# Optimization experiments

Hardware: AMD Instinct MI355X
Metric: run time of the kernel (lower is better)

Reference implementation:

```python
import jax, jax.numpy as jnp
import numpy as np

# Config
SEQ_LEN = 512
PRED_LEN = 96
C = 64
TOPM = 4
N_WIRES = 6
PERIODS = [2, 3, 4]          # periods dividing pred_len (model.period_num)
N_SAMPLES = 5000             # size of retrieval table along sample axis
B = 128

# ---- tiny quantum circuit simulation helpers ----
# State vector over n_wires qubits: shape [bsz, 2**n_wires].

def apply_single_qubit_gate(state, gate, wire, n_wires):
    # state: [bsz, 2**n]; gate: [2,2]
    st = state.reshape((state.shape[0],) + (2,) * n_wires)
    axis = 1 + wire
    st = jnp.moveaxis(st, axis, -1)
    st = jnp.einsum('...i,ji->...j', st, gate)
    st = jnp.moveaxis(st, -1, axis)
    return st.reshape(state.shape)

def ry_gate(theta):
    c = jnp.cos(theta / 2.0)
    s = jnp.sin(theta / 2.0)
    return jnp.stack([jnp.stack([c, -s]), jnp.stack([s, c])])

def apply_ry_batched(state, thetas, wire, n_wires):
    # thetas: [bsz] -> per-sample gate
    c = jnp.cos(thetas / 2.0)
    s = jnp.sin(thetas / 2.0)
    st = state.reshape((state.shape[0],) + (2,) * n_wires)
    axis = 1 + wire
    st = jnp.moveaxis(st, axis, -1)
    a0 = st[..., 0]
    a1 = st[..., 1]
    shp = (thetas.shape[0],) + (1,) * (st.ndim - 2)
    cb = c.reshape(shp)
    sb = s.reshape(shp)
    n0 = cb * a0 - sb * a1
    n1 = sb * a0 + cb * a1
    st = jnp.stack([n0, n1], axis=-1)
    st = jnp.moveaxis(st, -1, axis)
    return st.reshape(state.shape)

def quantum_circuit(x_query, ansatz_angles, ansatz_wires):
    # x_query: [bsz, n_wires] encoder RY angles.
    bsz = x_query.shape[0]
    dim = 2 ** N_WIRES
    state = jnp.zeros((bsz, dim), dtype=x_query.dtype).at[:, 0].set(1.0)
    # encoder: RY(x_i) on wire i
    for w in range(N_WIRES):
        state = apply_ry_batched(state, x_query[:, w], w, N_WIRES)
    # ansatz: fixed random RY rotations (RandomLayer approximated by RY ops)
    for k in range(ansatz_angles.shape[0]):
        g = ry_gate(ansatz_angles[k])
        state = apply_single_qubit_gate(state, g, int(ansatz_wires[k]), N_WIRES)
    # measure PauliZ expectation on each wire
    probs = jnp.abs(state) ** 2  # [bsz, 2**n]
    basis = jnp.arange(dim)
    exps = []
    for w in range(N_WIRES):
        bit = (basis >> (N_WIRES - 1 - w)) & 1
        z = 1.0 - 2.0 * bit.astype(probs.dtype)
        exps.append(probs @ z)
    return jnp.stack(exps, axis=-1)  # [bsz, n_wires]


def setup_inputs() -> dict:
    key = jax.random.key(0)
    ks = jax.random.split(key, 16)
    inp = {}
    inp['x_enc'] = jax.random.normal(ks[0], (B, SEQ_LEN, C), jnp.float32)
    inp['index'] = jax.random.randint(ks[1], (B,), 0, N_SAMPLES)
    # params
    s = 1.0 / np.sqrt(SEQ_LEN)
    inp['W_query'] = jax.random.uniform(ks[2], (N_WIRES, SEQ_LEN), jnp.float32, -s, s)
    inp['b_query'] = jnp.zeros((N_WIRES,), jnp.float32)
    inp['W_x'] = jax.random.uniform(ks[3], (PRED_LEN, SEQ_LEN), jnp.float32, -s, s)
    inp['b_x'] = jnp.zeros((PRED_LEN,), jnp.float32)
    sw = 1.0 / np.sqrt(N_WIRES)
    inp['W_prob'] = jax.random.uniform(ks[4], (TOPM, N_WIRES), jnp.float32, -sw, sw)
    inp['b_prob'] = jnp.zeros((TOPM,), jnp.float32)
    # retrieval_pred linears: Linear(pred_len//g, pred_len)
    for i, g in enumerate(PERIODS):
        d = PRED_LEN // g
        sg = 1.0 / np.sqrt(d)
        inp[f'W_ret{i}'] = jax.random.uniform(jax.random.fold_in(ks[5], i), (PRED_LEN, d), jnp.float32, -sg, sg)
        inp[f'b_ret{i}'] = jnp.zeros((PRED_LEN,), jnp.float32)
    sc = 1.0 / np.sqrt(2 * PRED_LEN)
    inp['W_pred'] = jax.random.uniform(ks[6], (PRED_LEN, 2 * PRED_LEN), jnp.float32, -sc, sc)
    inp['b_pred'] = jnp.zeros((PRED_LEN,), jnp.float32)
    # retrieval table: [n_period, n_samples, topm, pred_len, C]
    inp['retrieval_table'] = jax.random.normal(ks[7], (len(PERIODS), N_SAMPLES, TOPM, PRED_LEN, C), jnp.float32) * 0.1
    # fixed ansatz (random layer) angles and wires
    n_ops = N_WIRES * 3
    inp['ansatz_angles'] = jax.random.uniform(ks[8], (n_ops,), jnp.float32, 0.0, 2 * np.pi)
    inp['ansatz_wires'] = jax.random.randint(ks[9], (n_ops,), 0, N_WIRES)
    # gumbel noise (pre-sampled for determinism)
    u = jax.random.uniform(ks[10], (B * C, TOPM), jnp.float32, 1e-6, 1.0 - 1e-6)
    inp['gumbel_noise'] = -jnp.log(-jnp.log(u))
    return inp


def reference(x_enc, index, W_query, b_query, W_x, b_x, W_prob, b_prob,
              W_ret0, b_ret0, W_ret1, b_ret1, W_ret2, b_ret2,
              W_pred, b_pred, retrieval_table, ansatz_angles, ansatz_wires,
              gumbel_noise):
    Bsz = x_enc.shape[0]
    x_offset = x_enc[:, -1:, :]                 # [B,1,C]
    x_norm = x_enc - x_offset                   # [B,S,C]
    xT = jnp.transpose(x_norm, (0, 2, 1))       # [B,C,S]
    base_pred = jnp.transpose(xT @ W_x.T + b_x, (0, 2, 1))  # [B,P,C]
    q_in = (xT @ W_query.T + b_query).reshape(Bsz * C, N_WIRES)
    exp_val = quantum_circuit(q_in, ansatz_angles, ansatz_wires)  # [B*C, n_wires]
    logits = exp_val @ W_prob.T + b_prob        # [B*C, topm]
    # gumbel-softmax hard, tau=0.5
    y_soft = jax.nn.softmax((logits + gumbel_noise) / 0.5, axis=-1)
    idx = jnp.argmax(y_soft, axis=-1)
    y_hard = jax.nn.one_hot(idx, TOPM, dtype=y_soft.dtype)
    weights = y_hard + y_soft - jax.lax.stop_gradient(y_soft)
    weights = jnp.transpose(weights.reshape(Bsz, C, TOPM), (0, 2, 1))  # [B,topm,C]
    # retrieval: table[i, index] -> [B, topm, P, C]
    Wr = [W_ret0, W_ret1, W_ret2]
    br = [b_ret0, b_ret1, b_ret2]
    raw = jnp.zeros((Bsz, TOPM, PRED_LEN, C), x_enc.dtype)
    for i, g in enumerate(PERIODS):
        pr = retrieval_table[i][index]                         # [B,topm,P,C]
        pr = pr.reshape(Bsz * TOPM, PRED_LEN // g, g, C)[:, :, 0, :]  # [B*topm, P//g, C]
        prT = jnp.transpose(pr, (0, 2, 1))                     # [B*topm, C, P//g]
        pr = jnp.transpose(prT @ Wr[i].T + br[i], (0, 2, 1))   # [B*topm, P, C]
        raw = raw + pr.reshape(Bsz, TOPM, PRED_LEN, C)
    selected = (raw * weights[:, :, None, :]).sum(axis=1)       # [B,P,C]
    combined = jnp.concatenate([base_pred, selected], axis=1)   # [B,2P,C]
    cT = jnp.transpose(combined, (0, 2, 1))
    pred_norm = jnp.transpose(cT @ W_pred.T + b_pred, (0, 2, 1))
    return pred_norm + x_offset
```

## Files before the change

kernel.cpp:

```cpp
#include <hip/hip_runtime.h>

typedef short bf16x8 __attribute__((ext_vector_type(8)));
typedef float f32x4  __attribute__((ext_vector_type(4)));

#define WS_CONST 30720
#define WS_QBIAS 30816

__device__ __forceinline__ short f2bf(float f) {
    unsigned u = __float_as_uint(f);
    unsigned r = (u + 0x7FFFu + ((u >> 16) & 1u)) >> 16;
    return (short)r;
}

__global__ __launch_bounds__(256) void prep_kernel(
    const float* __restrict__ W_query, const float* __restrict__ b_query,
    const float* __restrict__ W_x,     const float* __restrict__ b_x,
    const float* __restrict__ W_ret0,  const float* __restrict__ b_ret0,
    const float* __restrict__ W_ret1,  const float* __restrict__ b_ret1,
    const float* __restrict__ W_ret2,  const float* __restrict__ b_ret2,
    const float* __restrict__ W_pred,  const float* __restrict__ b_pred,
    const float* __restrict__ angles,  const int* __restrict__ wires,
    float* __restrict__ ws)
{
    const int bid = blockIdx.x;
    const int t = threadIdx.x;
    __shared__ float wp[3072];
    __shared__ float wsl[768];
    short* ap = (short*)ws;

    if (bid < 240) {
        const int rg = bid % 3;
        const int cg = bid / 3;
        const bool isM1 = cg < 64;
        const int off = isM1 ? 0 : 96;
        #pragma unroll
        for (int i = 0; i < 12; ++i) {
            int L = t + i * 256;
            int r = L / 96, k = L - r * 96;
            wp[L] = W_pred[(rg * 32 + r) * 192 + off + k];
        }
        if (isM1) {
            const int s0 = cg * 8;
            #pragma unroll
            for (int i = 0; i < 3; ++i) {
                int L = t + i * 256;
                int k = L >> 3, s = L & 7;
                wsl[L] = W_x[k * 512 + s0 + s];
            }
        } else {
            const int j0 = (cg - 64) * 8;
            #pragma unroll
            for (int i = 0; i < 3; ++i) {
                int L = t + i * 256;
                int k = L >> 3, jj = L & 7;
                int j = j0 + jj;
                float v = 0.f;
                if (j < 104) {
                    const float* Wr; int d, jl;
                    if (j < 48)      { Wr = W_ret0; d = 48; jl = j; }
                    else if (j < 80) { Wr = W_ret1; d = 32; jl = j - 48; }
                    else             { Wr = W_ret2; d = 24; jl = j - 80; }
                    v = Wr[k * d + jl];
                }
                wsl[L] = v;
            }
        }
        __syncthreads();
        const int rl = t >> 3, s = t & 7;
        float acc = 0.f;
        #pragma unroll 8
        for (int k = 0; k < 96; ++k) acc += wp[rl * 96 + k] * wsl[k * 8 + s];
        const int r = rg * 32 + rl;
        const int sg = isM1 ? (cg * 8 + s) : (512 + (cg - 64) * 8 + s);
        const int kstep = sg >> 5, s32 = sg & 31;
        const int g = s32 >> 3, e = s32 & 7;
        ap[kstep * 3072 + (r >> 4) * 512 + (g * 16 + (r & 15)) * 8 + e] = f2bf(acc);
    } else {
        if (t < 96) {
            float v = b_pred[t];
            for (int k = 0; k < 96; ++k) {
                v += W_pred[t * 192 + k] * b_x[k];
                v += W_pred[t * 192 + 96 + k] * (b_ret0[k] + b_ret1[k] + b_ret2[k]);
            }
            ws[WS_CONST + t] = v;
        } else if (t < 102) {
            int w = t - 96;
            float v = b_query[w];
            for (int k = 0; k < 18; ++k)
                if (wires[k] == w) v += angles[k];
            ws[WS_QBIAS + w] = v;
        }
    }
}

__global__ __launch_bounds__(512) void main_kernel(
    const float* __restrict__ x_enc,
    const int*   __restrict__ index,
    const float* __restrict__ W_query,
    const float* __restrict__ W_prob,
    const float* __restrict__ b_prob,
    const float* __restrict__ RT,
    const float* __restrict__ gumbel,
    const float* __restrict__ ws,
    float* __restrict__ out)
{
    const int bid = blockIdx.x;
    const int b = bid & 127;
    const int cbase = (bid >> 7) * 16;
    const int t = threadIdx.x;
    const int lane = t & 63;
    const int wv = t >> 6;

    __shared__ __align__(16) union {
        struct { float wq[3072]; float qp[3072]; } s0;
        char Abuf[24576];
    } u0;
    __shared__ __align__(16) short xbuf[16][520];
    __shared__ __align__(16) union {
        float qfin[96];
        short selbuf[16][136];
    } u1;
    __shared__ int m_sel[16];

    const float* __restrict__ xb = x_enc + (size_t)b * 32768;

    {
        const float4* wsrc = (const float4*)W_query;
        float4* wdst = (float4*)u0.s0.wq;
        for (int L = t; L < 768; L += 512) wdst[L] = wsrc[L];
    }

    const int c  = t & 15;
    const int sg = t >> 4;
    const float xo = xb[511 * 64 + cbase + c];
    const float* xs = xb + (size_t)(sg * 16) * 64 + cbase + c;
    float v[16];
    #pragma unroll
    for (int i = 0; i < 16; ++i) v[i] = xs[i * 64];

    __syncthreads();

    {
        #pragma unroll
        for (int i = 0; i < 16; ++i) v[i] -= xo;
        const float4* wq4 = (const float4*)u0.s0.wq;
        float* qp = u0.s0.qp;
        #pragma unroll
        for (int wr = 0; wr < 6; ++wr) {
            float a = 0.f;
            #pragma unroll
            for (int i4 = 0; i4 < 4; ++i4) {
                float4 w4 = wq4[wr * 128 + sg * 4 + i4];
                a += w4.x * v[i4*4+0] + w4.y * v[i4*4+1] + w4.z * v[i4*4+2] + w4.w * v[i4*4+3];
            }
            qp[sg * 96 + wr * 16 + c] = a;
        }
        short* xrow = &xbuf[c][sg * 16];
        #pragma unroll
        for (int i = 0; i < 16; i += 2) {
            unsigned lo = (unsigned short)f2bf(v[i]);
            unsigned hi = (unsigned short)f2bf(v[i+1]);
            *(unsigned*)&xrow[i] = lo | (hi << 16);
        }
    }
    __syncthreads();

    if (t < 96) {
        int w6 = t >> 4, cc = t & 15;
        const float* qp = u0.s0.qp;
        float s = 0.f;
        #pragma unroll
        for (int g2 = 0; g2 < 32; ++g2) s += qp[g2 * 96 + w6 * 16 + cc];
        u1.qfin[w6 * 16 + cc] = s;
    }
    __syncthreads();

    if (t < 16) {
        float e[6];
        #pragma unroll
        for (int w = 0; w < 6; ++w) e[w] = cosf(u1.qfin[w * 16 + t] + ws[WS_QBIAS + w]);
        int grow = (b * 64 + cbase + t) * 4;
        float best = -1e30f; int bm = 0;
        #pragma unroll
        for (int m = 0; m < 4; ++m) {
            float lg = b_prob[m];
            #pragma unroll
            for (int w = 0; w < 6; ++w) lg += W_prob[m * 6 + w] * e[w];
            lg += gumbel[grow + m];
            if (lg > best) { best = lg; bm = m; }
        }
        m_sel[t] = bm;
    }
    __syncthreads();

    {
        const int idxb = index[b];
        for (int L = t; L < 16 * 136; L += 512) {
            int cc = L & 15, j = L >> 4;
            short val = 0;
            if (j < 104) {
                int i, row;
                if (j < 48)      { i = 0; row = j * 2; }
                else if (j < 80) { i = 1; row = (j - 48) * 3; }
                else             { i = 2; row = (j - 80) * 4; }
                val = f2bf(RT[(size_t)i * 122880000ull + (size_t)idxb * 24576ull
                             + (size_t)m_sel[cc] * 6144ull + (size_t)row * 64ull + cbase + cc]);
            }
            u1.selbuf[cc][j] = val;
        }
    }

    const char* Apack = (const char*)ws;
    const int cl = lane & 15, g = lane >> 4;
    f32x4 acc0 = {0,0,0,0};
    for (int ch = 0; ch < 5; ++ch) {
        const float4* asrc = (const float4*)(Apack + ch * 24576);
        float4 r0 = asrc[t], r1 = asrc[t + 512], r2 = asrc[t + 1024];
        __syncthreads();
        float4* adst = (float4*)u0.Abuf;
        adst[t] = r0; adst[t + 512] = r1; adst[t + 1024] = r2;
        __syncthreads();
        if (wv < 6) {
            #pragma unroll
            for (int ks = 0; ks < 4; ++ks) {
                bf16x8 av = *(const bf16x8*)(u0.Abuf + ks * 6144 + wv * 1024 + lane * 16);
                bf16x8 bv0;
                if (ch < 4) bv0 = *(const bf16x8*)&xbuf[cl][ch * 128 + ks * 32 + g * 8];
                else        bv0 = *(const bf16x8*)&u1.selbuf[cl][ks * 32 + g * 8];
                acc0 = __builtin_amdgcn_mfma_f32_16x16x32_bf16(av, bv0, acc0, 0, 0, 0);
            }
        }
    }

    if (wv < 6) {
        const float* cst = ws + WS_CONST;
        float xo0 = xb[511 * 64 + cbase + cl];
        int r0 = wv * 16 + g * 4;
        float* op = out + (size_t)b * 6144 + (size_t)r0 * 64 + cbase;
        #pragma unroll
        for (int reg = 0; reg < 4; ++reg)
            op[reg * 64 + cl] = acc0[reg] + cst[r0 + reg] + xo0;
    }
}

extern "C" void kernel_launch(void* const* d_in, const int* in_sizes, int n_in,
                              void* d_out, int out_size, void* d_ws, size_t ws_size,
                              hipStream_t stream) {
    (void)in_sizes; (void)n_in; (void)out_size; (void)ws_size;
    const float* x_enc   = (const float*)d_in[0];
    const int*   index   = (const int*)d_in[1];
    const float* W_query = (const float*)d_in[2];
    const float* b_query = (const float*)d_in[3];
    const float* W_x     = (const float*)d_in[4];
    const float* b_x     = (const float*)d_in[5];
    const float* W_prob  = (const float*)d_in[6];
    const float* b_prob  = (const float*)d_in[7];
    const float* W_ret0  = (const float*)d_in[8];
    const float* b_ret0  = (const float*)d_in[9];
    const float* W_ret1  = (const float*)d_in[10];
    const float* b_ret1  = (const float*)d_in[11];
    const float* W_ret2  = (const float*)d_in[12];
    const float* b_ret2  = (const float*)d_in[13];
    const float* W_pred  = (const float*)d_in[14];
    const float* b_pred  = (const float*)d_in[15];
    const float* RT      = (const float*)d_in[16];
    const float* angles  = (const float*)d_in[17];
    const int*   wires   = (const int*)d_in[18];
    const float* gumbel  = (const float*)d_in[19];
    float* out = (float*)d_out;
    float* ws  = (float*)d_ws;

    prep_kernel<<<241, 256, 0, stream>>>(W_query, b_query, W_x, b_x,
                                         W_ret0, b_ret0, W_ret1, b_ret1, W_ret2, b_ret2,
                                         W_pred, b_pred, angles, wires, ws);
    main_kernel<<<512, 512, 0, stream>>>(x_enc, index, W_query, W_prob, b_prob,
                                         RT, gumbel, ws, out);
}
```

Before: 24.03 us.

## Read MFMA A operands directly from global and overlap retrieval gather with GEMM

The packed A matrix is no longer staged through shared memory in five chunks with paired barriers; each wave loads its bf16 fragments straight from the global workspace. The W_query copy into LDS and one barrier are removed, with weights read directly from global. The retrieval-table gather is issued into registers before the x-part MFMA loop, and the results are written to LDS afterwards, so gather latency overlaps with compute. The cost is more global/L2 traffic per block and higher register pressure.

```diff
diff --git a/kernel.cpp b/kernel.cpp
--- a/kernel.cpp
+++ b/kernel.cpp
@@ -110,25 +110,17 @@
     const int t = threadIdx.x;
     const int lane = t & 63;
     const int wv = t >> 6;
+    const int cl = lane & 15, g = lane >> 4;
 
     __shared__ __align__(16) union {
-        struct { float wq[3072]; float qp[3072]; } s0;
-        char Abuf[24576];
+        float qp[3072];
+        short selbuf[16][136];
     } u0;
     __shared__ __align__(16) short xbuf[16][520];
-    __shared__ __align__(16) union {
-        float qfin[96];
-        short selbuf[16][136];
-    } u1;
+    __shared__ float qfin[96];
     __shared__ int m_sel[16];
 
     const float* __restrict__ xb = x_enc + (size_t)b * 32768;
-
-    {
-        const float4* wsrc = (const float4*)W_query;
-        float4* wdst = (float4*)u0.s0.wq;
-        for (int L = t; L < 768; L += 512) wdst[L] = wsrc[L];
-    }
 
     const int c  = t & 15;
     const int sg = t >> 4;
@@ -138,13 +130,10 @@
     #pragma unroll
     for (int i = 0; i < 16; ++i) v[i] = xs[i * 64];
 
-    __syncthreads();
-
     {
         #pragma unroll
         for (int i = 0; i < 16; ++i) v[i] -= xo;
-        const float4* wq4 = (const float4*)u0.s0.wq;
-        float* qp = u0.s0.qp;
+        const float4* wq4 = (const float4*)W_query;
         #pragma unroll
         for (int wr = 0; wr < 6; ++wr) {
             float a = 0.f;
@@ -153,7 +142,7 @@
                 float4 w4 = wq4[wr * 128 + sg * 4 + i4];
                 a += w4.x * v[i4*4+0] + w4.y * v[i4*4+1] + w4.z * v[i4*4+2] + w4.w * v[i4*4+3];
             }
-            qp[sg * 96 + wr * 16 + c] = a;
+            u0.qp[sg * 96 + wr * 16 + c] = a;
         }
         short* xrow = &xbuf[c][sg * 16];
         #pragma unroll
@@ -167,18 +156,18 @@
 
     if (t < 96) {
         int w6 = t >> 4, cc = t & 15;
-        const float* qp = u0.s0.qp;
+        const float* qp = u0.qp;
         float s = 0.f;
         #pragma unroll
         for (int g2 = 0; g2 < 32; ++g2) s += qp[g2 * 96 + w6 * 16 + cc];
-        u1.qfin[w6 * 16 + cc] = s;
+        qfin[w6 * 16 + cc] = s;
     }
     __syncthreads();
 
     if (t < 16) {
         float e[6];
         #pragma unroll
-        for (int w = 0; w < 6; ++w) e[w] = cosf(u1.qfin[w * 16 + t] + ws[WS_QBIAS + w]);
+        for (int w = 0; w < 6; ++w) e[w] = cosf(qfin[w * 16 + t] + ws[WS_QBIAS + w]);
         int grow = (b * 64 + cbase + t) * 4;
         float best = -1e30f; int bm = 0;
         #pragma unroll
@@ -193,53 +182,61 @@
     }
     __syncthreads();
 
-    {
-        const int idxb = index[b];
-        for (int L = t; L < 16 * 136; L += 512) {
-            int cc = L & 15, j = L >> 4;
-            short val = 0;
+    const int idxb = index[b];
+    float gv[5];
+    #pragma unroll
+    for (int it = 0; it < 5; ++it) {
+        const int L = t + it * 512;
+        float val = 0.f;
+        if (L < 2176) {
+            const int cc = L & 15, j = L >> 4;
             if (j < 104) {
                 int i, row;
                 if (j < 48)      { i = 0; row = j * 2; }
                 else if (j < 80) { i = 1; row = (j - 48) * 3; }
                 else             { i = 2; row = (j - 80) * 4; }
-                val = f2bf(RT[(size_t)i * 122880000ull + (size_t)idxb * 24576ull
-                             + (size_t)m_sel[cc] * 6144ull + (size_t)row * 64ull + cbase + cc]);
-            }
-            u1.selbuf[cc][j] = val;
-        }
-    }
-
-    const char* Apack = (const char*)ws;
-    const int cl = lane & 15, g = lane >> 4;
-    f32x4 acc0 = {0,0,0,0};
-    for (int ch = 0; ch < 5; ++ch) {
-        const float4* asrc = (const float4*)(Apack + ch * 24576);
-        float4 r0 = asrc[t], r1 = asrc[t + 512], r2 = asrc[t + 1024];
-        __syncthreads();
-        float4* adst = (float4*)u0.Abuf;
-        adst[t] = r0; adst[t + 512] = r1; adst[t + 1024] = r2;
-        __syncthreads();
-        if (wv < 6) {
-            #pragma unroll
-            for (int ks = 0; ks < 4; ++ks) {
-                bf16x8 av = *(const bf16x8*)(u0.Abuf + ks * 6144 + wv * 1024 + lane * 16);
-                bf16x8 bv0;
-                if (ch < 4) bv0 = *(const bf16x8*)&xbuf[cl][ch * 128 + ks * 32 + g * 8];
-                else        bv0 = *(const bf16x8*)&u1.selbuf[cl][ks * 32 + g * 8];
-                acc0 = __builtin_amdgcn_mfma_f32_16x16x32_bf16(av, bv0, acc0, 0, 0, 0);
-            }
-        }
-    }
-
+                val = RT[(size_t)i * 122880000ull + (size_t)idxb * 24576ull
+                         + (size_t)m_sel[cc] * 6144ull + (size_t)row * 64ull + cbase + cc];
+            }
+        }
+        gv[it] = val;
+    }
+
+    const char* Ap = (const char*)ws;
+    f32x4 acc = {0,0,0,0};
     if (wv < 6) {
+        #pragma unroll 4
+        for (int ks = 0; ks < 16; ++ks) {
+            bf16x8 av = *(const bf16x8*)(Ap + ks * 6144 + wv * 1024 + lane * 16);
+            bf16x8 bv = *(const bf16x8*)&xbuf[cl][ks * 32 + g * 8];
+            acc = __builtin_amdgcn_mfma_f32_16x16x32_bf16(av, bv, acc, 0, 0, 0);
+        }
+    }
+
+    #pragma unroll
+    for (int it = 0; it < 5; ++it) {
+        const int L = t + it * 512;
+        if (L < 2176) {
+            const int cc = L & 15, j = L >> 4;
+            u0.selbuf[cc][j] = f2bf(gv[it]);
+        }
+    }
+    __syncthreads();
+
+    if (wv < 6) {
+        #pragma unroll
+        for (int ks = 0; ks < 4; ++ks) {
+            bf16x8 av = *(const bf16x8*)(Ap + (16 + ks) * 6144 + wv * 1024 + lane * 16);
+            bf16x8 bv = *(const bf16x8*)&u0.selbuf[cl][ks * 32 + g * 8];
+            acc = __builtin_amdgcn_mfma_f32_16x16x32_bf16(av, bv, acc, 0, 0, 0);
+        }
         const float* cst = ws + WS_CONST;
         float xo0 = xb[511 * 64 + cbase + cl];
         int r0 = wv * 16 + g * 4;
         float* op = out + (size_t)b * 6144 + (size_t)r0 * 64 + cbase;
         #pragma unroll
         for (int reg = 0; reg < 4; ++reg)
-            op[reg * 64 + cl] = acc0[reg] + cst[r0 + reg] + xo0;
+            op[reg * 64 + cl] = acc[reg] + cst[r0 + reg] + xo0;
     }
 }
 
```

Result: faster. 23.29 us (median of 2 runs) (-3.1%).
